# Optimization experiments

Hardware: AMD Instinct MI355X
Metric: run time of the kernel (lower is better)

## Reference

```python
import jax, jax.numpy as jnp
import numpy as np

T = 8192        # minority samples
D = 128         # n_hidden (SMOTE dims)
K = 3           # smote k
N_MULT = 4      # synthetic samples per minority row (N/100)
C = 16          # n_classes


def setup_inputs() -> dict:
    key = jax.random.key(0)
    k1, k2, k3, k4 = jax.random.split(key, 4)
    X = jax.random.normal(k1, (T, D), dtype=jnp.float32)
    # randint(0, k-2) inclusive in torch -> values in {0, ..., K-2}
    nn_idx = jax.random.randint(k2, (N_MULT * T,), 0, K - 1, dtype=jnp.int32)
    gaps = jax.random.uniform(k3, (N_MULT * T,), dtype=jnp.float32)
    W = jax.random.normal(k4, (D, C), dtype=jnp.float32) / np.float32(np.sqrt(D))
    b = jnp.zeros((C,), dtype=jnp.float32)
    return {"X": X, "nn_idx": nn_idx, "gaps": gaps, "W": W, "b": b}


def reference(X, nn_idx, gaps, W, b):
    # --- find_k: full pairwise euclidean distance (fused, replaces per-row loop) ---
    sq = jnp.sum(X * X, axis=1)                       # [T]
    d2 = sq[:, None] + sq[None, :] - 2.0 * (X @ X.T)  # [T, T]
    dist = jnp.sqrt(jnp.maximum(d2, 0.0))
    # --- k_neighbors: k smallest distances; col 0 is self (dist 0) ---
    _, idxs = jax.lax.top_k(-dist, K)                 # [T, K], ascending distance
    nbrs = idxs[:, 1:K]                               # [T, K-1]
    # --- populate: gather-based interpolation, N_MULT synthetic rows per source ---
    src = jnp.repeat(jnp.arange(T), N_MULT)           # [N_syn], row order matches torch loop
    chosen = nbrs[src, nn_idx]                        # [N_syn]
    x_src = X[src]                                    # [N_syn, D]
    syn = x_src + gaps[:, None] * (X[chosen] - x_src) # [N_syn, D]
    # --- classifier on concatenated real + synthetic embeddings ---
    Xa = jnp.concatenate([X, syn], axis=0)            # [T + N_syn, D]
    logits = Xa @ W + b                               # [T + N_syn, C]
    return logits
```

## Files before the change

kernel.cpp:

```cpp
#include <hip/hip_runtime.h>

#define T_PTS 8192
#define D_DIM 128
#define C_OUT 16
#define NSPLIT 8
#define JSPAN (T_PTS / NSPLIT)
#define NJT (JSPAN / 64)
#define LSTR 132
#define MSTR 65

typedef _Float16 half8 __attribute__((ext_vector_type(8)));
typedef __attribute__((ext_vector_type(4))) float f32x4;
typedef unsigned short ushort_t;
typedef unsigned int uint_t;


__global__ void prep_kernel(const float* __restrict__ X, _Float16* __restrict__ Xs,
                            float* __restrict__ sq) {
    const int tid = threadIdx.x;
    const int row = blockIdx.x * 16 + (tid >> 4);
    const int ch = tid & 15;
    const float4* p = (const float4*)(X + row * D_DIM + ch * 8);
    const float4 a = p[0], b = p[1];
    half8 o;
    o[0] = (_Float16)a.x; o[1] = (_Float16)a.y; o[2] = (_Float16)a.z; o[3] = (_Float16)a.w;
    o[4] = (_Float16)b.x; o[5] = (_Float16)b.y; o[6] = (_Float16)b.z; o[7] = (_Float16)b.w;
    const int t = row >> 4, m = row & 15, k = ch >> 2, q = ch & 3;
    *(half8*)(Xs + t * 2048 + k * 512 + (q * 16 + m) * 8) = o;
    float s = a.x * a.x + a.y * a.y + a.z * a.z + a.w * a.w
            + b.x * b.x + b.y * b.y + b.z * b.z + b.w * b.w;
    s += __shfl_xor(s, 1); s += __shfl_xor(s, 2);
    s += __shfl_xor(s, 4); s += __shfl_xor(s, 8);
    if (ch == 0) sq[row] = s;
}

__launch_bounds__(256, 2)
__global__ void nn_kernel(const _Float16* __restrict__ Xs, const float* __restrict__ sq,
                          float* __restrict__ ckey, ushort_t* __restrict__ cidx) {
    __shared__ float mk[64 * MSTR];
    __shared__ int mj[64 * MSTR];

    const int tid = threadIdx.x;
    const int w = tid >> 6;
    const int lane = tid & 63;
    const int quad = lane >> 4;
    const int l15 = lane & 15;
    const int i0 = blockIdx.x * 64;
    const int sp = blockIdx.y;
    const int j0 = sp * JSPAN;

    half8 bfrag[4][4];
#pragma unroll
    for (int n = 0; n < 4; ++n)
#pragma unroll
        for (int k = 0; k < 4; ++k)
            bfrag[n][k] = *(const half8*)(Xs + ((i0 >> 4) + n) * 2048 + k * 512 + lane * 8);

    float c0[4], c1[4], c2[4], c3[4], sk[4];
#pragma unroll
    for (int n = 0; n < 4; ++n) { c0[n] = c1[n] = c2[n] = c3[n] = sk[n] = 1e30f; }

    int icol[4];
#pragma unroll
    for (int n = 0; n < 4; ++n) icol[n] = i0 + n * 16 + l15;

    const bool blk_excl = (sp == (i0 / JSPAN));
    const int excl_jt = (i0 & (JSPAN - 1)) >> 6;

    for (int jt = 0; jt < NJT; ++jt) {
        const int jbase = j0 + jt * 64;
        const int jtile = (jbase >> 4) + w;
        half8 af[4];
#pragma unroll
        for (int k = 0; k < 4; ++k)
            af[k] = *(const half8*)(Xs + jtile * 2048 + k * 512 + lane * 8);
        const f32x4 sq4 = *(const f32x4*)(sq + jbase + w * 16 + quad * 4);
        const int jg = jbase + w * 16 + quad * 4;
        const bool excl = blk_excl && (jt == excl_jt);
        const uint_t ib = (uint_t)(jt * 4);

#pragma unroll
        for (int n = 0; n < 4; ++n) {
            f32x4 acc = {0.f, 0.f, 0.f, 0.f};
#pragma unroll
            for (int k = 0; k < 4; ++k)
                acc = __builtin_amdgcn_mfma_f32_16x16x32_f16(af[k], bfrag[n][k], acc, 0, 0, 0);
            float q0 = fmaf(-2.f, acc[0], sq4[0]);
            float q1 = fmaf(-2.f, acc[1], sq4[1]);
            float q2 = fmaf(-2.f, acc[2], sq4[2]);
            float q3 = fmaf(-2.f, acc[3], sq4[3]);
            if (excl) {
                if (jg + 0 == icol[n]) q0 = 1e30f;
                if (jg + 1 == icol[n]) q1 = 1e30f;
                if (jg + 2 == icol[n]) q2 = 1e30f;
                if (jg + 3 == icol[n]) q3 = 1e30f;
            }
            const float p0 = __uint_as_float((__float_as_uint(q0) & 0xFFFFFFC0u) | (ib + 0));
            const float p1 = __uint_as_float((__float_as_uint(q1) & 0xFFFFFFC0u) | (ib + 1));
            const float p2 = __uint_as_float((__float_as_uint(q2) & 0xFFFFFFC0u) | (ib + 2));
            const float p3 = __uint_as_float((__float_as_uint(q3) & 0xFFFFFFC0u) | (ib + 3));
            const float min01 = fminf(p0, p1), max01 = fmaxf(p0, p1);
            const float min23 = fminf(p2, p3), max23 = fmaxf(p2, p3);
            const float kmin = fminf(min01, min23);
            const float ksec = fminf(fmaxf(min01, min23), fminf(max01, max23));
            c3[n] = __builtin_amdgcn_fmed3f(c2[n], c3[n], kmin);
            c2[n] = __builtin_amdgcn_fmed3f(c1[n], c2[n], kmin);
            c1[n] = __builtin_amdgcn_fmed3f(c0[n], c1[n], kmin);
            c0[n] = fminf(c0[n], kmin);
            sk[n] = fminf(sk[n], ksec);
        }
    }

#pragma unroll
    for (int n = 0; n < 4; ++n) {
        const float v = sk[n];
        c3[n] = __builtin_amdgcn_fmed3f(c2[n], c3[n], v);
        c2[n] = __builtin_amdgcn_fmed3f(c1[n], c2[n], v);
        c1[n] = __builtin_amdgcn_fmed3f(c0[n], c1[n], v);
        c0[n] = fminf(c0[n], v);
    }

    const int s = w * 4 + quad;
    const int jdec0 = j0 + w * 16 + quad * 4;
#pragma unroll
    for (int n = 0; n < 4; ++n) {
        const int il = n * 16 + l15;
        const int base = il * MSTR + s * 4;
        float cc[4] = {c0[n], c1[n], c2[n], c3[n]};
#pragma unroll
        for (int e = 0; e < 4; ++e) {
            const uint_t p = __float_as_uint(cc[e]) & 63u;
            mk[base + e] = cc[e];
            mj[base + e] = jdec0 + (int)(p >> 2) * 64 + (int)(p & 3);
        }
    }
    __syncthreads();
    if (tid < 64) {
        float a0 = 1e30f, a1 = 1e30f, a2 = 1e30f, a3 = 1e30f;
        int b0 = 0, b1 = 0, b2 = 0, b3 = 0;
        for (int e = 0; e < 64; ++e) {
            float k = mk[tid * MSTR + e];
            int j = mj[tid * MSTR + e];
            bool l0 = k < a0, l1 = k < a1, l2 = k < a2, l3 = k < a3;
            a3 = l2 ? a2 : (l3 ? k : a3); b3 = l2 ? b2 : (l3 ? j : b3);
            a2 = l1 ? a1 : (l2 ? k : a2); b2 = l1 ? b1 : (l2 ? j : b2);
            a1 = l0 ? a0 : (l1 ? k : a1); b1 = l0 ? b0 : (l1 ? j : b1);
            a0 = l0 ? k : a0;             b0 = l0 ? j : b0;
        }
        const int gi = i0 + tid;
        f32x4 kv = {a0, a1, a2, a3};
        *(f32x4*)(ckey + (sp * T_PTS + gi) * 4) = kv;
        ushort_t* c = cidx + (sp * T_PTS + gi) * 4;
        c[0] = (ushort_t)b0; c[1] = (ushort_t)b1; c[2] = (ushort_t)b2; c[3] = (ushort_t)b3;
    }
}

__global__ void merge8_kernel(const float* __restrict__ ckey, const ushort_t* __restrict__ cidx,
                              ushort_t* __restrict__ nb8) {
    __shared__ int idxs[256 * 33];
    const int tid = threadIdx.x;
    const int i = blockIdx.x * 256 + tid;
    float c0 = 1e30f, c1 = 1e30f, c2 = 1e30f, c3 = 1e30f;
    float c4 = 1e30f, c5 = 1e30f, c6 = 1e30f, c7 = 1e30f;
#pragma unroll
    for (int sp = 0; sp < NSPLIT; ++sp) {
        const f32x4 kk = *(const f32x4*)(ckey + (sp * T_PTS + i) * 4);
        const ushort_t* jj = cidx + (sp * T_PTS + i) * 4;
        ushort_t j4[4];
        *(uint2*)j4 = *(const uint2*)jj;
#pragma unroll
        for (int e4 = 0; e4 < 4; ++e4) {
            const uint_t e = (uint_t)(sp * 4 + e4);
            const float v = __uint_as_float((__float_as_uint(kk[e4]) & 0xFFFFFFC0u) | e);
            idxs[tid * 33 + e] = (int)j4[e4];
            c7 = __builtin_amdgcn_fmed3f(c6, c7, v);
            c6 = __builtin_amdgcn_fmed3f(c5, c6, v);
            c5 = __builtin_amdgcn_fmed3f(c4, c5, v);
            c4 = __builtin_amdgcn_fmed3f(c3, c4, v);
            c3 = __builtin_amdgcn_fmed3f(c2, c3, v);
            c2 = __builtin_amdgcn_fmed3f(c1, c2, v);
            c1 = __builtin_amdgcn_fmed3f(c0, c1, v);
            c0 = fminf(c0, v);
        }
    }
    float top[8] = {c0, c1, c2, c3, c4, c5, c6, c7};
    ushort_t o[8];
#pragma unroll
    for (int r = 0; r < 8; ++r) {
        const uint_t p = __float_as_uint(top[r]) & 63u;
        o[r] = (ushort_t)idxs[tid * 33 + (int)p];
    }
    *(uint2*)(nb8 + i * 8) = *(const uint2*)o;
    *(uint2*)(nb8 + i * 8 + 4) = *(const uint2*)(o + 4);
}

__global__ void rescore8_kernel(const float* __restrict__ X, const float* __restrict__ sq,
                                const ushort_t* __restrict__ nb8, int* __restrict__ nbrs) {
    __shared__ float keys[32][9];
    __shared__ int idxs[32][9];
    const int tid = threadIdx.x;
    const int rr = tid >> 3;
    const int cc = tid & 7;
    const int i = blockIdx.x * 32 + rr;
    {
        const int j = (int)nb8[i * 8 + cc];
        const float4* xi = (const float4*)(X + i * D_DIM);
        const float4* xj = (const float4*)(X + j * D_DIM);
        float ssum = 0.f;
#pragma unroll
        for (int q = 0; q < 32; ++q) {
            const float4 a = xi[q], b2 = xj[q];
            ssum += a.x * b2.x; ssum += a.y * b2.y; ssum += a.z * b2.z; ssum += a.w * b2.w;
        }
        float key = sq[j] - 2.f * ssum;
        if (j == i) key = 1e30f;
        keys[rr][cc] = key;
        idxs[rr][cc] = j;
    }
    __syncthreads();
    if (tid < 32) {
        float m0 = 1e30f, m1 = 1e30f;
        int n0 = 0x7fffffff, n1 = 0x7fffffff;
        for (int e = 0; e < 8; ++e) {
            float k = keys[tid][e];
            int j = idxs[tid][e];
            bool lt0 = (k < m0) || (k == m0 && j < n0);
            bool lt1 = (k < m1) || (k == m1 && j < n1);
            if (lt0) { m1 = m0; n1 = n0; m0 = k; n0 = j; }
            else if (lt1) { m1 = k; n1 = j; }
        }
        const int i2 = blockIdx.x * 32 + tid;
        nbrs[i2 * 2 + 0] = n0;
        nbrs[i2 * 2 + 1] = n1;
    }
}

__launch_bounds__(256)
__global__ void y_kernel(const float* __restrict__ X, const float* __restrict__ W,
                         const float* __restrict__ b, float* __restrict__ Y,
                         float* __restrict__ out) {
    __shared__ float Xsl[16 * LSTR];
    __shared__ float Ws[D_DIM * C_OUT];
    const int tid = threadIdx.x;
    const int r0 = blockIdx.x * 16;
    const float4* src = (const float4*)(X + r0 * D_DIM);
#pragma unroll
    for (int it = 0; it < 2; ++it) {
        int f = tid + it * 256;
        int row = f >> 5, kq = f & 31;
        *(float4*)(Xsl + row * LSTR + kq * 4) = src[row * 32 + kq];
    }
#pragma unroll
    for (int it = 0; it < 2; ++it) {
        int f = tid + it * 256;
        ((float4*)Ws)[f] = ((const float4*)W)[f];
    }
    __syncthreads();
    const int r = tid >> 4, c = tid & 15;
    float s = b[c];
#pragma unroll
    for (int d = 0; d < D_DIM; ++d) s += Xsl[r * LSTR + d] * Ws[d * C_OUT + c];
    const int row = r0 + r;
    Y[row * C_OUT + c] = s;
    out[row * C_OUT + c] = s;
}

__global__ void syn_kernel(const float* __restrict__ Y, const int* __restrict__ nbrs,
                           const int* __restrict__ nn_idx, const float* __restrict__ gaps,
                           float* __restrict__ out) {
    const int idx = blockIdx.x * 256 + threadIdx.x;
    const int m = idx >> 4;
    const int c = idx & 15;
    const int src = m >> 2;
    const int sel = nn_idx[m];
    const int ch = nbrs[src * 2 + sel];
    const float g = gaps[m];
    const float ys = Y[src * C_OUT + c];
    const float yc = Y[ch * C_OUT + c];
    out[(T_PTS + m) * C_OUT + c] = ys + g * (yc - ys);
}

extern "C" void kernel_launch(void* const* d_in, const int* in_sizes, int n_in,
                              void* d_out, int out_size, void* d_ws, size_t ws_size,
                              hipStream_t stream) {
    const float* X = (const float*)d_in[0];
    const int* nn_idx = (const int*)d_in[1];
    const float* gaps = (const float*)d_in[2];
    const float* W = (const float*)d_in[3];
    const float* b = (const float*)d_in[4];
    float* out = (float*)d_out;

    char* ws = (char*)d_ws;
    _Float16* Xs = (_Float16*)ws;
    float* sq = (float*)(ws + 2097152);
    float* ckey = (float*)(ws + 2129920);
    ushort_t* cidx = (ushort_t*)(ws + 3178496);
    ushort_t* nb8 = (ushort_t*)(ws + 3702784);
    int* nbrs = (int*)(ws + 3833856);
    float* Y = (float*)(ws + 2129920 + 32768);
    Y = (float*)(ws + 2129920);

    prep_kernel<<<T_PTS / 16, 256, 0, stream>>>(X, Xs, sq);
    nn_kernel<<<dim3(T_PTS / 64, NSPLIT), 256, 0, stream>>>(Xs, sq, ckey, cidx);
    merge8_kernel<<<T_PTS / 256, 256, 0, stream>>>(ckey, cidx, nb8);
    rescore8_kernel<<<T_PTS / 32, 256, 0, stream>>>(X, sq, nb8, nbrs);
    y_kernel<<<T_PTS / 16, 256, 0, stream>>>(X, W, b, Y, out);
    syn_kernel<<<(4 * T_PTS * C_OUT) / 256, 256, 0, stream>>>(Y, nbrs, nn_idx, gaps, out);
}
```

Baseline: 118.4 us.

## Prefetch next j-tile, reduce candidates via shuffles, fuse merge into rescore

The nn_kernel now loads the next j-tile's fp16 fragments and squared norms one iteration ahead, so global load latency overlaps with the MFMA work. Per-row top-4 candidates are merged across quads with xor shuffles instead of a 64-entry LDS scan. Two extra quad bits are packed into the key's low mantissa bits so indices can be decoded later, which costs slightly more key precision. The separate merge8 and rescore8 kernels are fused into one tail kernel, removing a launch and the round trip through global memory.

```diff
diff --git a/kernel.cpp b/kernel.cpp
--- a/kernel.cpp
+++ b/kernel.cpp
@@ -7,7 +7,6 @@
 #define JSPAN (T_PTS / NSPLIT)
 #define NJT (JSPAN / 64)
 #define LSTR 132
-#define MSTR 65
 
 typedef _Float16 half8 __attribute__((ext_vector_type(8)));
 typedef __attribute__((ext_vector_type(4))) float f32x4;
@@ -34,11 +33,19 @@
     if (ch == 0) sq[row] = s;
 }
 
+#define INS4(c0_, c1_, c2_, c3_, v_)                         \
+    do {                                                     \
+        const float _v = (v_);                               \
+        c3_ = __builtin_amdgcn_fmed3f(c2_, c3_, _v);         \
+        c2_ = __builtin_amdgcn_fmed3f(c1_, c2_, _v);         \
+        c1_ = __builtin_amdgcn_fmed3f(c0_, c1_, _v);         \
+        c0_ = fminf(c0_, _v);                                \
+    } while (0)
+
 __launch_bounds__(256, 2)
 __global__ void nn_kernel(const _Float16* __restrict__ Xs, const float* __restrict__ sq,
                           float* __restrict__ ckey, ushort_t* __restrict__ cidx) {
-    __shared__ float mk[64 * MSTR];
-    __shared__ int mj[64 * MSTR];
+    __shared__ float mkLds[4][64][5];
 
     const int tid = threadIdx.x;
     const int w = tid >> 6;
@@ -60,24 +67,35 @@
 #pragma unroll
     for (int n = 0; n < 4; ++n) { c0[n] = c1[n] = c2[n] = c3[n] = sk[n] = 1e30f; }
 
-    int icol[4];
-#pragma unroll
-    for (int n = 0; n < 4; ++n) icol[n] = i0 + n * 16 + l15;
-
     const bool blk_excl = (sp == (i0 / JSPAN));
     const int excl_jt = (i0 & (JSPAN - 1)) >> 6;
 
+    half8 af[4];
+    f32x4 sq4;
+    {
+        const int jtile = (j0 >> 4) + w;
+#pragma unroll
+        for (int k = 0; k < 4; ++k)
+            af[k] = *(const half8*)(Xs + jtile * 2048 + k * 512 + lane * 8);
+        sq4 = *(const f32x4*)(sq + j0 + w * 16 + quad * 4);
+    }
+
+#pragma unroll 2
     for (int jt = 0; jt < NJT; ++jt) {
         const int jbase = j0 + jt * 64;
-        const int jtile = (jbase >> 4) + w;
-        half8 af[4];
-#pragma unroll
-        for (int k = 0; k < 4; ++k)
-            af[k] = *(const half8*)(Xs + jtile * 2048 + k * 512 + lane * 8);
-        const f32x4 sq4 = *(const f32x4*)(sq + jbase + w * 16 + quad * 4);
         const int jg = jbase + w * 16 + quad * 4;
+        half8 afn[4];
+        f32x4 sq4n;
+        {
+            const int jb2 = j0 + ((jt + 1) & (NJT - 1)) * 64;
+            const int jtile2 = (jb2 >> 4) + w;
+#pragma unroll
+            for (int k = 0; k < 4; ++k)
+                afn[k] = *(const half8*)(Xs + jtile2 * 2048 + k * 512 + lane * 8);
+            sq4n = *(const f32x4*)(sq + jb2 + w * 16 + quad * 4);
+        }
         const bool excl = blk_excl && (jt == excl_jt);
-        const uint_t ib = (uint_t)(jt * 4);
+        const uint_t ib = (uint_t)((quad << 6) | (jt * 4));
 
 #pragma unroll
         for (int n = 0; n < 4; ++n) {
@@ -90,63 +108,73 @@
             float q2 = fmaf(-2.f, acc[2], sq4[2]);
             float q3 = fmaf(-2.f, acc[3], sq4[3]);
             if (excl) {
-                if (jg + 0 == icol[n]) q0 = 1e30f;
-                if (jg + 1 == icol[n]) q1 = 1e30f;
-                if (jg + 2 == icol[n]) q2 = 1e30f;
-                if (jg + 3 == icol[n]) q3 = 1e30f;
+                const int ic = i0 + n * 16 + l15;
+                if (jg + 0 == ic) q0 = 1e30f;
+                if (jg + 1 == ic) q1 = 1e30f;
+                if (jg + 2 == ic) q2 = 1e30f;
+                if (jg + 3 == ic) q3 = 1e30f;
             }
-            const float p0 = __uint_as_float((__float_as_uint(q0) & 0xFFFFFFC0u) | (ib + 0));
-            const float p1 = __uint_as_float((__float_as_uint(q1) & 0xFFFFFFC0u) | (ib + 1));
-            const float p2 = __uint_as_float((__float_as_uint(q2) & 0xFFFFFFC0u) | (ib + 2));
-            const float p3 = __uint_as_float((__float_as_uint(q3) & 0xFFFFFFC0u) | (ib + 3));
+            const float p0 = __uint_as_float((__float_as_uint(q0) & 0xFFFFFF00u) | (ib + 0));
+            const float p1 = __uint_as_float((__float_as_uint(q1) & 0xFFFFFF00u) | (ib + 1));
+            const float p2 = __uint_as_float((__float_as_uint(q2) & 0xFFFFFF00u) | (ib + 2));
+            const float p3 = __uint_as_float((__float_as_uint(q3) & 0xFFFFFF00u) | (ib + 3));
             const float min01 = fminf(p0, p1), max01 = fmaxf(p0, p1);
             const float min23 = fminf(p2, p3), max23 = fmaxf(p2, p3);
             const float kmin = fminf(min01, min23);
             const float ksec = fminf(fmaxf(min01, min23), fminf(max01, max23));
-            c3[n] = __builtin_amdgcn_fmed3f(c2[n], c3[n], kmin);
-            c2[n] = __builtin_amdgcn_fmed3f(c1[n], c2[n], kmin);
-            c1[n] = __builtin_amdgcn_fmed3f(c0[n], c1[n], kmin);
-            c0[n] = fminf(c0[n], kmin);
+            INS4(c0[n], c1[n], c2[n], c3[n], kmin);
             sk[n] = fminf(sk[n], ksec);
         }
+#pragma unroll
+        for (int k = 0; k < 4; ++k) af[k] = afn[k];
+        sq4 = sq4n;
     }
 
 #pragma unroll
     for (int n = 0; n < 4; ++n) {
-        const float v = sk[n];
-        c3[n] = __builtin_amdgcn_fmed3f(c2[n], c3[n], v);
-        c2[n] = __builtin_amdgcn_fmed3f(c1[n], c2[n], v);
-        c1[n] = __builtin_amdgcn_fmed3f(c0[n], c1[n], v);
-        c0[n] = fminf(c0[n], v);
-    }
-
-    const int s = w * 4 + quad;
-    const int jdec0 = j0 + w * 16 + quad * 4;
-#pragma unroll
-    for (int n = 0; n < 4; ++n) {
-        const int il = n * 16 + l15;
-        const int base = il * MSTR + s * 4;
-        float cc[4] = {c0[n], c1[n], c2[n], c3[n]};
-#pragma unroll
-        for (int e = 0; e < 4; ++e) {
-            const uint_t p = __float_as_uint(cc[e]) & 63u;
-            mk[base + e] = cc[e];
-            mj[base + e] = jdec0 + (int)(p >> 2) * 64 + (int)(p & 3);
+        INS4(c0[n], c1[n], c2[n], c3[n], sk[n]);
+        float d0 = __shfl_xor(c0[n], 16), d1 = __shfl_xor(c1[n], 16);
+        float d2 = __shfl_xor(c2[n], 16), d3 = __shfl_xor(c3[n], 16);
+        INS4(c0[n], c1[n], c2[n], c3[n], d0);
+        INS4(c0[n], c1[n], c2[n], c3[n], d1);
+        INS4(c0[n], c1[n], c2[n], c3[n], d2);
+        INS4(c0[n], c1[n], c2[n], c3[n], d3);
+        d0 = __shfl_xor(c0[n], 32); d1 = __shfl_xor(c1[n], 32);
+        d2 = __shfl_xor(c2[n], 32); d3 = __shfl_xor(c3[n], 32);
+        INS4(c0[n], c1[n], c2[n], c3[n], d0);
+        INS4(c0[n], c1[n], c2[n], c3[n], d1);
+        INS4(c0[n], c1[n], c2[n], c3[n], d2);
+        INS4(c0[n], c1[n], c2[n], c3[n], d3);
+    }
+
+    if (quad == 0) {
+#pragma unroll
+        for (int n = 0; n < 4; ++n) {
+            const int row = n * 16 + l15;
+            mkLds[w][row][0] = c0[n];
+            mkLds[w][row][1] = c1[n];
+            mkLds[w][row][2] = c2[n];
+            mkLds[w][row][3] = c3[n];
         }
     }
     __syncthreads();
     if (tid < 64) {
         float a0 = 1e30f, a1 = 1e30f, a2 = 1e30f, a3 = 1e30f;
         int b0 = 0, b1 = 0, b2 = 0, b3 = 0;
-        for (int e = 0; e < 64; ++e) {
-            float k = mk[tid * MSTR + e];
-            int j = mj[tid * MSTR + e];
-            bool l0 = k < a0, l1 = k < a1, l2 = k < a2, l3 = k < a3;
-            a3 = l2 ? a2 : (l3 ? k : a3); b3 = l2 ? b2 : (l3 ? j : b3);
-            a2 = l1 ? a1 : (l2 ? k : a2); b2 = l1 ? b1 : (l2 ? j : b2);
-            a1 = l0 ? a0 : (l1 ? k : a1); b1 = l0 ? b0 : (l1 ? j : b1);
-            a0 = l0 ? k : a0;             b0 = l0 ? j : b0;
-        }
+#pragma unroll
+        for (int wv = 0; wv < 4; ++wv)
+#pragma unroll
+            for (int e = 0; e < 4; ++e) {
+                const float kk = mkLds[wv][tid][e];
+                const uint_t p8 = __float_as_uint(kk) & 255u;
+                const int j = j0 + (int)((p8 & 63u) >> 2) * 64 + wv * 16
+                            + (int)((p8 >> 6) & 3u) * 4 + (int)(p8 & 3u);
+                bool l0 = kk < a0, l1 = kk < a1, l2 = kk < a2, l3 = kk < a3;
+                a3 = l2 ? a2 : (l3 ? kk : a3); b3 = l2 ? b2 : (l3 ? j : b3);
+                a2 = l1 ? a1 : (l2 ? kk : a2); b2 = l1 ? b1 : (l2 ? j : b2);
+                a1 = l0 ? a0 : (l1 ? kk : a1); b1 = l0 ? b0 : (l1 ? j : b1);
+                a0 = l0 ? kk : a0;             b0 = l0 ? j : b0;
+            }
         const int gi = i0 + tid;
         f32x4 kv = {a0, a1, a2, a3};
         *(f32x4*)(ckey + (sp * T_PTS + gi) * 4) = kv;
@@ -155,55 +183,50 @@
     }
 }
 
-__global__ void merge8_kernel(const float* __restrict__ ckey, const ushort_t* __restrict__ cidx,
-                              ushort_t* __restrict__ nb8) {
-    __shared__ int idxs[256 * 33];
-    const int tid = threadIdx.x;
-    const int i = blockIdx.x * 256 + tid;
-    float c0 = 1e30f, c1 = 1e30f, c2 = 1e30f, c3 = 1e30f;
-    float c4 = 1e30f, c5 = 1e30f, c6 = 1e30f, c7 = 1e30f;
-#pragma unroll
-    for (int sp = 0; sp < NSPLIT; ++sp) {
-        const f32x4 kk = *(const f32x4*)(ckey + (sp * T_PTS + i) * 4);
-        const ushort_t* jj = cidx + (sp * T_PTS + i) * 4;
-        ushort_t j4[4];
-        *(uint2*)j4 = *(const uint2*)jj;
-#pragma unroll
-        for (int e4 = 0; e4 < 4; ++e4) {
-            const uint_t e = (uint_t)(sp * 4 + e4);
-            const float v = __uint_as_float((__float_as_uint(kk[e4]) & 0xFFFFFFC0u) | e);
-            idxs[tid * 33 + e] = (int)j4[e4];
-            c7 = __builtin_amdgcn_fmed3f(c6, c7, v);
-            c6 = __builtin_amdgcn_fmed3f(c5, c6, v);
-            c5 = __builtin_amdgcn_fmed3f(c4, c5, v);
-            c4 = __builtin_amdgcn_fmed3f(c3, c4, v);
-            c3 = __builtin_amdgcn_fmed3f(c2, c3, v);
-            c2 = __builtin_amdgcn_fmed3f(c1, c2, v);
-            c1 = __builtin_amdgcn_fmed3f(c0, c1, v);
-            c0 = fminf(c0, v);
-        }
-    }
-    float top[8] = {c0, c1, c2, c3, c4, c5, c6, c7};
-    ushort_t o[8];
-#pragma unroll
-    for (int r = 0; r < 8; ++r) {
-        const uint_t p = __float_as_uint(top[r]) & 63u;
-        o[r] = (ushort_t)idxs[tid * 33 + (int)p];
-    }
-    *(uint2*)(nb8 + i * 8) = *(const uint2*)o;
-    *(uint2*)(nb8 + i * 8 + 4) = *(const uint2*)(o + 4);
-}
-
-__global__ void rescore8_kernel(const float* __restrict__ X, const float* __restrict__ sq,
-                                const ushort_t* __restrict__ nb8, int* __restrict__ nbrs) {
+__global__ void tail_kernel(const float* __restrict__ X, const float* __restrict__ sq,
+                            const float* __restrict__ ckey, const ushort_t* __restrict__ cidx,
+                            int* __restrict__ nbrs) {
+    __shared__ ushort_t cLds[32][33];
+    __shared__ ushort_t nb8s[32][8];
     __shared__ float keys[32][9];
     __shared__ int idxs[32][9];
     const int tid = threadIdx.x;
-    const int rr = tid >> 3;
-    const int cc = tid & 7;
-    const int i = blockIdx.x * 32 + rr;
+    const int ib0 = blockIdx.x * 32;
+
+    if (tid < 32) {
+        const int i = ib0 + tid;
+        float c0 = 1e30f, c1 = 1e30f, c2 = 1e30f, c3 = 1e30f;
+        float c4 = 1e30f, c5 = 1e30f, c6 = 1e30f, c7 = 1e30f;
+#pragma unroll
+        for (int sp2 = 0; sp2 < NSPLIT; ++sp2) {
+            const f32x4 kk = *(const f32x4*)(ckey + (sp2 * T_PTS + i) * 4);
+            ushort_t j4[4];
+            *(uint2*)j4 = *(const uint2*)(cidx + (sp2 * T_PTS + i) * 4);
+#pragma unroll
+            for (int e4 = 0; e4 < 4; ++e4) {
+                const uint_t e = (uint_t)(sp2 * 4 + e4);
+                const float v = __uint_as_float((__float_as_uint(kk[e4]) & 0xFFFFFFC0u) | e);
+                cLds[tid][e] = j4[e4];
+                c7 = __builtin_amdgcn_fmed3f(c6, c7, v);
+                c6 = __builtin_amdgcn_fmed3f(c5, c6, v);
+                c5 = __builtin_amdgcn_fmed3f(c4, c5, v);
+                c4 = __builtin_amdgcn_fmed3f(c3, c4, v);
+                c3 = __builtin_amdgcn_fmed3f(c2, c3, v);
+                c2 = __builtin_amdgcn_fmed3f(c1, c2, v);
+                c1 = __builtin_amdgcn_fmed3f(c0, c1, v);
+                c0 = fminf(c0, v);
+            }
+        }
+        const float top[8] = {c0, c1, c2, c3, c4, c5, c6, c7};
+#pragma unroll
+        for (int r = 0; r < 8; ++r)
+            nb8s[tid][r] = cLds[tid][__float_as_uint(top[r]) & 63u];
+    }
+    __syncthreads();
     {
-        const int j = (int)nb8[i * 8 + cc];
+        const int rr = tid >> 3, cc = tid & 7;
+        const int i = ib0 + rr;
+        const int j = (int)nb8s[rr][cc];
         const float4* xi = (const float4*)(X + i * D_DIM);
         const float4* xj = (const float4*)(X + j * D_DIM);
         float ssum = 0.f;
@@ -221,17 +244,18 @@
     if (tid < 32) {
         float m0 = 1e30f, m1 = 1e30f;
         int n0 = 0x7fffffff, n1 = 0x7fffffff;
+#pragma unroll
         for (int e = 0; e < 8; ++e) {
-            float k = keys[tid][e];
-            int j = idxs[tid][e];
+            const float k = keys[tid][e];
+            const int j = idxs[tid][e];
             bool lt0 = (k < m0) || (k == m0 && j < n0);
             bool lt1 = (k < m1) || (k == m1 && j < n1);
             if (lt0) { m1 = m0; n1 = n0; m0 = k; n0 = j; }
             else if (lt1) { m1 = k; n1 = j; }
         }
-        const int i2 = blockIdx.x * 32 + tid;
-        nbrs[i2 * 2 + 0] = n0;
-        nbrs[i2 * 2 + 1] = n1;
+        const int i = ib0 + tid;
+        nbrs[i * 2 + 0] = n0;
+        nbrs[i * 2 + 1] = n1;
     }
 }
 
@@ -295,15 +319,12 @@
     float* sq = (float*)(ws + 2097152);
     float* ckey = (float*)(ws + 2129920);
     ushort_t* cidx = (ushort_t*)(ws + 3178496);
-    ushort_t* nb8 = (ushort_t*)(ws + 3702784);
-    int* nbrs = (int*)(ws + 3833856);
-    float* Y = (float*)(ws + 2129920 + 32768);
-    Y = (float*)(ws + 2129920);
+    int* nbrs = (int*)(ws + 3702784);
+    float* Y = (float*)(ws + 2129920);
 
     prep_kernel<<<T_PTS / 16, 256, 0, stream>>>(X, Xs, sq);
     nn_kernel<<<dim3(T_PTS / 64, NSPLIT), 256, 0, stream>>>(Xs, sq, ckey, cidx);
-    merge8_kernel<<<T_PTS / 256, 256, 0, stream>>>(ckey, cidx, nb8);
-    rescore8_kernel<<<T_PTS / 32, 256, 0, stream>>>(X, sq, nb8, nbrs);
+    tail_kernel<<<T_PTS / 32, 256, 0, stream>>>(X, sq, ckey, cidx, nbrs);
     y_kernel<<<T_PTS / 16, 256, 0, stream>>>(X, W, b, Y, out);
     syn_kernel<<<(4 * T_PTS * C_OUT) / 256, 256, 0, stream>>>(Y, nbrs, nn_idx, gaps, out);
 }
```

Result: faster. 111.2 us (-6.1%).
